# Optimization experiments

Measured on AMD Instinct MI355X. Metric: run time of the kernel, lower is better.

Reference implementation:

```python
import jax, jax.numpy as jnp
import numpy as np

B, T, C = 2, 2048, 2048
H, N = 32, 64
EPS_GN = 1e-5 * 8**2  # GroupNorm eps = 1e-5 * head_size_divisor**2


def setup_inputs() -> dict:
    key = jax.random.key(0)
    ks = iter(jax.random.split(key, 40))
    nk = lambda: next(ks)
    u = lambda shape: jax.random.uniform(nk(), shape, jnp.float32)
    n = lambda shape, s: jax.random.normal(nk(), shape, jnp.float32) * s
    return dict(
        x=jax.random.normal(nk(), (B, T, C), jnp.float32),
        v_first=jax.random.normal(nk(), (B, T, C), jnp.float32),
        x_r=u((1, 1, C)), x_w=u((1, 1, C)), x_k=u((1, 1, C)),
        x_v=u((1, 1, C)), x_a=u((1, 1, C)), x_g=u((1, 1, C)),
        w0=(jnp.linspace(-7.0, -2.0, C) + 0.5).reshape(1, 1, C).astype(jnp.float32),
        w1=n((C, 64), 0.02), w2=n((64, C), 0.1),
        a0=jnp.zeros((1, 1, C), jnp.float32), a1=n((C, 64), 0.02), a2=n((64, C), 0.1),
        v0=jnp.ones((1, 1, C), jnp.float32), v1=n((C, 32), 0.02), v2=n((32, C), 0.1),
        g1=n((C, 128), 0.02), g2=n((128, C), 0.1),
        k_k=jnp.full((1, 1, C), 0.85, jnp.float32),
        k_a=jnp.ones((1, 1, C), jnp.float32),
        r_k=n((H, N), 0.1),
        W_r=n((C, C), C ** -0.5), W_k=n((C, C), 0.1 * C ** -0.5),
        W_v=n((C, C), C ** -0.5), W_o=n((C, C), 0.02),
        gn_w=jnp.ones((C,), jnp.float32), gn_b=jnp.zeros((C,), jnp.float32),
    )


def _rwkv7(r, w, k, v, z, b):
    # all inputs [B,T,H,N]; state S [B,H,N_v,N_k] per head
    decay = jnp.exp(-jnp.exp(w))

    def step(S, xs):
        rt, dt, kt, vt, zt, bt = xs  # each [B,H,N]
        sa = jnp.einsum('bhij,bhj->bhi', S, zt)
        S = (S * dt[:, :, None, :]
             + sa[..., None] * bt[:, :, None, :]
             + vt[..., None] * kt[:, :, None, :])
        y = jnp.einsum('bhij,bhj->bhi', S, rt)
        return S, y

    xs = tuple(jnp.moveaxis(t, 1, 0) for t in (r, decay, k, v, z, b))
    S0 = jnp.zeros((r.shape[0], r.shape[2], N, N), r.dtype)
    _, ys = jax.lax.scan(step, S0, xs)
    return jnp.moveaxis(ys, 0, 1)  # [B,T,H,N]


def reference(x, v_first, x_r, x_w, x_k, x_v, x_a, x_g,
              w0, w1, w2, a0, a1, a2, v0, v1, v2, g1, g2,
              k_k, k_a, r_k, W_r, W_k, W_v, W_o, gn_w, gn_b):
    # time shift: x_{t-1} (zero at t=0) minus x
    xx = jnp.concatenate([jnp.zeros_like(x[:, :1]), x[:, :-1]], axis=1) - x
    xr = x + xx * x_r
    xw = x + xx * x_w
    xk = x + xx * x_k
    xv = x + xx * x_v
    xa = x + xx * x_a
    xg = x + xx * x_g

    r = xr @ W_r.T
    w = -jax.nn.softplus(-(w0 + jnp.tanh(xw @ w1) @ w2)) - 0.5  # log-decay in (-inf,-0.5)
    k = xk @ W_k.T
    v = xv @ W_v.T
    # layer_id != 0: blend with first-layer value
    v = v + (v_first - v) * jax.nn.sigmoid(v0 + (xv @ v1) @ v2)
    a = jax.nn.sigmoid(a0 + (xa @ a1) @ a2)
    g = jax.nn.sigmoid(xg @ g1) @ g2

    kk = (k * k_k).reshape(B, T, H, N)
    kk = kk / jnp.maximum(jnp.linalg.norm(kk, axis=-1, keepdims=True), 1e-12)
    k = k * (1.0 + (a - 1.0) * k_a)

    rh = r.reshape(B, T, H, N)
    kh = k.reshape(B, T, H, N)
    vh = v.reshape(B, T, H, N)
    ah = a.reshape(B, T, H, N)
    y = _rwkv7(rh, w.reshape(B, T, H, N), kh, vh, -kk, kk * ah)  # [B,T,H,N]

    # GroupNorm(H groups) over each head of each (b,t) row
    mu = y.mean(-1, keepdims=True)
    var = y.var(-1, keepdims=True)
    yn = ((y - mu) / jnp.sqrt(var + EPS_GN)).reshape(B, T, C) * gn_w + gn_b

    bonus = ((rh * kh * r_k).sum(-1, keepdims=True) * vh).reshape(B, T, C)
    out = ((yn + bonus) * g) @ W_o.T
    return (out, v_first)
```

## Files before the change

### kernel.cpp

```cpp
#include <hip/hip_runtime.h>
#include <stdint.h>

typedef unsigned short u16;
typedef unsigned int u32;

#define B_ 2
#define T_ 2048
#define C_ 2048
#define H_ 32
#define M_ (B_*T_)
static const size_t MC = (size_t)M_ * C_;

typedef __attribute__((ext_vector_type(8))) short s16x8;
typedef __attribute__((ext_vector_type(4))) float f32x4;

__device__ __forceinline__ u16 f2bf(float f) {
  union { float f; u32 u; } v; v.f = f;
  u32 r = v.u + 0x7FFFu + ((v.u >> 16) & 1u);
  return (u16)(r >> 16);
}
__device__ __forceinline__ float bits2f(u32 u) {
  union { u32 u; float f; } v; v.u = u; return v.f;
}
__device__ __forceinline__ float bf2f(u16 h) { return bits2f(((u32)h) << 16); }
__device__ __forceinline__ float sigm(float x) { return 1.0f / (1.0f + expf(-x)); }

__device__ __forceinline__ float wsum64(float x) {
  x += __shfl_xor(x, 32);
  x += __shfl_xor(x, 16);
  x += __shfl_xor(x, 8);
  x += __shfl_xor(x, 4);
  x += __shfl_xor(x, 2);
  x += __shfl_xor(x, 1);
  return x;
}

#define GL2LDS(g, l) __builtin_amdgcn_global_load_lds( \
    (const __attribute__((address_space(1))) u32*)(g), \
    (__attribute__((address_space(3))) u32*)(l), 16, 0, 0)

__global__ void __launch_bounds__(256) gemm128f(const u16* __restrict__ A, const u16* __restrict__ Bm,
                                                float* __restrict__ Cm, int M, int N, int K) {
  __shared__ u16 As[128 * 32];
  __shared__ u16 Bs[128 * 32];
  const int tid = threadIdx.x;
  const int w = tid >> 6, l = tid & 63;
  const int wm = w >> 1, wn = w & 1;
  const int bm = blockIdx.x, bn = blockIdx.y;

  const int row0 = tid >> 2, kq0 = tid & 3;
  const u16* ag0 = A + (size_t)(bm * 128 + row0) * K + kq0 * 8;
  const u16* ag1 = ag0 + (size_t)64 * K;
  const u16* bg0 = Bm + (size_t)(bn * 128 + row0) * K + kq0 * 8;
  const u16* bg1 = bg0 + (size_t)64 * K;
  u16* al0 = &As[w * 512];
  u16* al1 = &As[2048 + w * 512];
  u16* bl0 = &Bs[w * 512];
  u16* bl1 = &Bs[2048 + w * 512];

  const int lrow = l & 15, lko = (l >> 4) * 8;
  const u16* Ars = &As[(wm * 64 + lrow) * 32 + lko];
  const u16* Brs = &Bs[(wn * 64 + lrow) * 32 + lko];

  f32x4 acc[4][4] = {};
  for (int k0 = 0; k0 < K; k0 += 32) {
    __syncthreads();
    GL2LDS(ag0, al0); GL2LDS(ag1, al1);
    GL2LDS(bg0, bl0); GL2LDS(bg1, bl1);
    ag0 += 32; ag1 += 32; bg0 += 32; bg1 += 32;
    __syncthreads();
    s16x8 af[4], bf[4];
#pragma unroll
    for (int m = 0; m < 4; ++m) af[m] = *(const s16x8*)(Ars + m * 16 * 32);
#pragma unroll
    for (int n = 0; n < 4; ++n) bf[n] = *(const s16x8*)(Brs + n * 16 * 32);
#pragma unroll
    for (int m = 0; m < 4; ++m)
#pragma unroll
      for (int n = 0; n < 4; ++n)
        acc[m][n] = __builtin_amdgcn_mfma_f32_16x16x32_bf16(af[m], bf[n], acc[m][n], 0, 0, 0);
  }
  const int crow0 = bm * 128 + wm * 64 + (l >> 4) * 4;
  const int ccol0 = bn * 128 + wn * 64 + (l & 15);
#pragma unroll
  for (int m = 0; m < 4; ++m)
#pragma unroll
    for (int rr = 0; rr < 4; ++rr) {
      const int row = crow0 + m * 16 + rr;
      float* cp = Cm + (size_t)row * N + ccol0;
#pragma unroll
      for (int n = 0; n < 4; ++n) cp[n * 16] = acc[m][n][rr];
    }
}

struct GTab4 {
  const u16* A[4]; const u16* Bm[4]; u16* Cm[4]; int K[4];
};
__global__ void __launch_bounds__(256) gemm128z(GTab4 t, int M, int N) {
  __shared__ u16 As[128 * 32];
  __shared__ u16 Bs[128 * 32];
  const int z = blockIdx.z;
  const u16* A = t.A[z];
  const u16* Bm = t.Bm[z];
  u16* Cm = t.Cm[z];
  const int K = t.K[z];
  const int tid = threadIdx.x;
  const int w = tid >> 6, l = tid & 63;
  const int wm = w >> 1, wn = w & 1;
  const int bm = blockIdx.x, bn = blockIdx.y;

  const int row0 = tid >> 2, kq0 = tid & 3;
  const u16* ag0 = A + (size_t)(bm * 128 + row0) * K + kq0 * 8;
  const u16* ag1 = ag0 + (size_t)64 * K;
  const u16* bg0 = Bm + (size_t)(bn * 128 + row0) * K + kq0 * 8;
  const u16* bg1 = bg0 + (size_t)64 * K;
  u16* al0 = &As[w * 512];
  u16* al1 = &As[2048 + w * 512];
  u16* bl0 = &Bs[w * 512];
  u16* bl1 = &Bs[2048 + w * 512];

  const int lrow = l & 15, lko = (l >> 4) * 8;
  const u16* Ars = &As[(wm * 64 + lrow) * 32 + lko];
  const u16* Brs = &Bs[(wn * 64 + lrow) * 32 + lko];

  f32x4 acc[4][4] = {};
  for (int k0 = 0; k0 < K; k0 += 32) {
    __syncthreads();
    GL2LDS(ag0, al0); GL2LDS(ag1, al1);
    GL2LDS(bg0, bl0); GL2LDS(bg1, bl1);
    ag0 += 32; ag1 += 32; bg0 += 32; bg1 += 32;
    __syncthreads();
    s16x8 af[4], bf[4];
#pragma unroll
    for (int m = 0; m < 4; ++m) af[m] = *(const s16x8*)(Ars + m * 16 * 32);
#pragma unroll
    for (int n = 0; n < 4; ++n) bf[n] = *(const s16x8*)(Brs + n * 16 * 32);
#pragma unroll
    for (int m = 0; m < 4; ++m)
#pragma unroll
      for (int n = 0; n < 4; ++n)
        acc[m][n] = __builtin_amdgcn_mfma_f32_16x16x32_bf16(af[m], bf[n], acc[m][n], 0, 0, 0);
  }
  const int crow0 = bm * 128 + wm * 64 + (l >> 4) * 4;
  const int ccol0 = bn * 128 + wn * 64 + (l & 15);
#pragma unroll
  for (int m = 0; m < 4; ++m)
#pragma unroll
    for (int rr = 0; rr < 4; ++rr) {
      const int row = crow0 + m * 16 + rr;
      u16* cp = Cm + (size_t)row * N + ccol0;
#pragma unroll
      for (int n = 0; n < 4; ++n) cp[n * 16] = f2bf(acc[m][n][rr]);
    }
}

__global__ void __launch_bounds__(256) gemm_lora1(
    const u16* __restrict__ xwb, const u16* __restrict__ xab,
    const u16* __restrict__ xvb, const u16* __restrict__ xgb,
    const u16* __restrict__ w1t, const u16* __restrict__ a1t,
    const u16* __restrict__ v1t, const u16* __restrict__ g1t,
    float* __restrict__ hw, float* __restrict__ ha,
    float* __restrict__ hv, float* __restrict__ hg) {
  __shared__ u16 As[128 * 32];
  __shared__ u16 Bs[32 * 32];
  const int tid = threadIdx.x;
  const int w = tid >> 6, l = tid & 63;
  const int bm = blockIdx.x, g = blockIdx.y, z = blockIdx.z;

  const u16* A; const u16* Bm; float* Cm; int ldc, coloff;
  switch (g) {
    case 0:  A = xwb; Bm = w1t;             Cm = hw; ldc = 64;  coloff = 0;  break;
    case 1:  A = xwb; Bm = w1t + 32 * 2048; Cm = hw; ldc = 64;  coloff = 32; break;
    case 2:  A = xab; Bm = a1t;             Cm = ha; ldc = 64;  coloff = 0;  break;
    case 3:  A = xab; Bm = a1t + 32 * 2048; Cm = ha; ldc = 64;  coloff = 32; break;
    case 4:  A = xvb; Bm = v1t;             Cm = hv; ldc = 32;  coloff = 0;  break;
    default: {
      int gg = g - 5;
      A = xgb; Bm = g1t + (size_t)gg * 32 * 2048; Cm = hg; ldc = 128; coloff = gg * 32;
    }
  }
  A += z * 1024; Bm += z * 1024;
  Cm += (size_t)z * M_ * ldc;

  const int row0 = tid >> 2, kq0 = tid & 3;
  const u16* ag0 = A + (size_t)(bm * 128 + row0) * 2048 + kq0 * 8;
  const u16* ag1 = ag0 + (size_t)64 * 2048;
  u16* al0 = &As[w * 512];
  u16* al1 = &As[2048 + w * 512];
  const int bc = (w & 1) * 64 + l;
  const u16* bg0 = Bm + (size_t)(bc >> 2) * 2048 + (bc & 3) * 8;
  u16* bl0 = &Bs[(w & 1) * 512];

  const int lrow = l & 15, lko = (l >> 4) * 8;
  const u16* Ars = &As[(w * 32 + lrow) * 32 + lko];
  const u16* Brs = &Bs[lrow * 32 + lko];

  f32x4 acc[2][2] = {};
  for (int k0 = 0; k0 < 1024; k0 += 32) {
    __syncthreads();
    GL2LDS(ag0, al0); GL2LDS(ag1, al1);
    if (w < 2) GL2LDS(bg0, bl0);
    ag0 += 32; ag1 += 32; bg0 += 32;
    __syncthreads();
    s16x8 af[2], bf[2];
    af[0] = *(const s16x8*)(Ars);
    af[1] = *(const s16x8*)(Ars + 16 * 32);
    bf[0] = *(const s16x8*)(Brs);
    bf[1] = *(const s16x8*)(Brs + 16 * 32);
#pragma unroll
    for (int m = 0; m < 2; ++m)
#pragma unroll
      for (int n = 0; n < 2; ++n)
        acc[m][n] = __builtin_amdgcn_mfma_f32_16x16x32_bf16(af[m], bf[n], acc[m][n], 0, 0, 0);
  }
  const int crow0 = bm * 128 + w * 32 + (l >> 4) * 4;
  const int ccol0 = coloff + (l & 15);
#pragma unroll
  for (int m = 0; m < 2; ++m)
#pragma unroll
    for (int rr = 0; rr < 4; ++rr) {
      const int row = crow0 + m * 16 + rr;
      float* cp = Cm + (size_t)row * ldc + ccol0;
      cp[0] = acc[m][0][rr];
      cp[16] = acc[m][1][rr];
    }
}

__global__ void __launch_bounds__(256) act_lora(
    const float* __restrict__ hw, const float* __restrict__ ha,
    const float* __restrict__ hv, const float* __restrict__ hg,
    u16* __restrict__ hwb, u16* __restrict__ hab,
    u16* __restrict__ hvb, u16* __restrict__ hgb) {
  int gid = blockIdx.x * 256 + threadIdx.x;
  const int S0 = M_ * 64, S1 = M_ * 64, S2 = M_ * 32, S3 = M_ * 128;
  float v; u16* out; int idx;
  if (gid < S0) { idx = gid; v = tanhf(hw[idx] + hw[idx + S0]); out = hwb; }
  else if (gid < S0 + S1) { idx = gid - S0; v = ha[idx] + ha[idx + S1]; out = hab; }
  else if (gid < S0 + S1 + S2) { idx = gid - S0 - S1; v = hv[idx] + hv[idx + S2]; out = hvb; }
  else { idx = gid - S0 - S1 - S2; v = sigm(hg[idx] + hg[idx + S3]); out = hgb; }
  out[idx] = f2bf(v);
}

__global__ void __launch_bounds__(256) prep_mix(const float* __restrict__ x,
    const float* __restrict__ mr, const float* __restrict__ mw, const float* __restrict__ mk,
    const float* __restrict__ mv, const float* __restrict__ ma, const float* __restrict__ mg,
    u16* __restrict__ xrb, u16* __restrict__ xwb, u16* __restrict__ xkb,
    u16* __restrict__ xvb, u16* __restrict__ xab, u16* __restrict__ xgb) {
  int gid = blockIdx.x * 256 + threadIdx.x;
  int row = gid >> 8;
  int col = (gid & 255) << 3;
  size_t base = (size_t)row * C_ + col;
  float xv[8], dx[8];
  *(float4*)&xv[0] = *(const float4*)(x + base);
  *(float4*)&xv[4] = *(const float4*)(x + base + 4);
  if ((row & (T_ - 1)) == 0) {
#pragma unroll
    for (int j = 0; j < 8; ++j) dx[j] = -xv[j];
  } else {
    float xp[8];
    *(float4*)&xp[0] = *(const float4*)(x + base - C_);
    *(float4*)&xp[4] = *(const float4*)(x + base - C_ + 4);
#pragma unroll
    for (int j = 0; j < 8; ++j) dx[j] = xp[j] - xv[j];
  }
#define EMIT(dst, mixp) { \
    float4 m0 = *(const float4*)(mixp + col); \
    float4 m1 = *(const float4*)(mixp + col + 4); \
    float o0 = xv[0] + dx[0] * m0.x, o1 = xv[1] + dx[1] * m0.y; \
    float o2 = xv[2] + dx[2] * m0.z, o3 = xv[3] + dx[3] * m0.w; \
    float o4 = xv[4] + dx[4] * m1.x, o5 = xv[5] + dx[5] * m1.y; \
    float o6 = xv[6] + dx[6] * m1.z, o7 = xv[7] + dx[7] * m1.w; \
    uint4 pk; \
    pk.x = (u32)f2bf(o0) | ((u32)f2bf(o1) << 16); \
    pk.y = (u32)f2bf(o2) | ((u32)f2bf(o3) << 16); \
    pk.z = (u32)f2bf(o4) | ((u32)f2bf(o5) << 16); \
    pk.w = (u32)f2bf(o6) | ((u32)f2bf(o7) << 16); \
    *(uint4*)(dst + base) = pk; }
  EMIT(xrb, mr) EMIT(xwb, mw) EMIT(xkb, mk) EMIT(xvb, mv) EMIT(xab, ma) EMIT(xgb, mg)
#undef EMIT
}

__global__ void __launch_bounds__(256) convbf8x4(
    const float* __restrict__ i0, const float* __restrict__ i1,
    const float* __restrict__ i2, const float* __restrict__ i3,
    u16* __restrict__ o0, u16* __restrict__ o1, u16* __restrict__ o2, u16* __restrict__ o3) {
  const float* in; u16* out;
  switch (blockIdx.y) {
    case 0: in = i0; out = o0; break;
    case 1: in = i1; out = o1; break;
    case 2: in = i2; out = o2; break;
    default: in = i3; out = o3;
  }
  int gid = blockIdx.x * 256 + threadIdx.x;
  size_t b = (size_t)gid * 8;
  float4 a0 = *(const float4*)(in + b), a1 = *(const float4*)(in + b + 4);
  uint4 pk;
  pk.x = (u32)f2bf(a0.x) | ((u32)f2bf(a0.y) << 16);
  pk.y = (u32)f2bf(a0.z) | ((u32)f2bf(a0.w) << 16);
  pk.z = (u32)f2bf(a1.x) | ((u32)f2bf(a1.y) << 16);
  pk.w = (u32)f2bf(a1.z) | ((u32)f2bf(a1.w) << 16);
  *(uint4*)(out + b) = pk;
}

__global__ void __launch_bounds__(256) tconvbf8(
    const float* __restrict__ w1, const float* __restrict__ a1,
    const float* __restrict__ v1, const float* __restrict__ g1,
    const float* __restrict__ w2, const float* __restrict__ a2,
    const float* __restrict__ v2, const float* __restrict__ g2,
    u16* __restrict__ w1t, u16* __restrict__ a1t, u16* __restrict__ v1t, u16* __restrict__ g1t,
    u16* __restrict__ w2t, u16* __restrict__ a2t, u16* __restrict__ v2t, u16* __restrict__ g2t) {
  const float* in; u16* out; int R, Cc;
  switch (blockIdx.y) {
    case 0: in = w1; out = w1t; R = 2048; Cc = 64; break;
    case 1: in = a1; out = a1t; R = 2048; Cc = 64; break;
    case 2: in = v1; out = v1t; R = 2048; Cc = 32; break;
    case 3: in = g1; out = g1t; R = 2048; Cc = 128; break;
    case 4: in = w2; out = w2t; R = 64; Cc = 2048; break;
    case 5: in = a2; out = a2t; R = 64; Cc = 2048; break;
    case 6: in = v2; out = v2t; R = 32; Cc = 2048; break;
    default: in = g2; out = g2t; R = 128; Cc = 2048;
  }
  int gid = blockIdx.x * 256 + threadIdx.x;
  if (gid >= R * Cc) return;
  int i = gid % R, j = gid / R;
  out[gid] = f2bf(in[(size_t)i * Cc + j]);
}

__global__ void __launch_bounds__(256) scan_prep(
    const u16* __restrict__ rb, u16* __restrict__ kb, u16* __restrict__ vb,
    const u16* __restrict__ dwb, u16* __restrict__ dab, u16* __restrict__ dvbb,
    const float* __restrict__ v_first,
    const float* __restrict__ a0, const float* __restrict__ v0, const float* __restrict__ w0,
    const float* __restrict__ k_k, const float* __restrict__ k_a, const float* __restrict__ r_k,
    float* __restrict__ dec, u16* __restrict__ bonus) {
  int rh = blockIdx.x * 4 + (threadIdx.x >> 6);
  int n = threadIdx.x & 63;
  int h = rh & (H_ - 1);
  size_t idx = (size_t)rh * 64 + n;
  int c = h * 64 + n;
  float kv = bf2f(kb[idx]), dav = bf2f(dab[idx]), dwv = bf2f(dwb[idx]);
  float dvv = bf2f(dvbb[idx]), vv = bf2f(vb[idx]);
  float vf = v_first[idx], rv = bf2f(rb[idx]);
  float av = sigm(a0[c] + dav);
  float kkv = kv * k_k[c];
  float ss = wsum64(kkv * kkv);
  float kkn = kkv / fmaxf(sqrtf(ss), 1e-12f);
  float k2 = kv * (1.f + (av - 1.f) * k_a[c]);
  float w_ = w0[c] + dwv;
  float wl = -log1pf(expf(-w_)) - 0.5f;
  float decf = expf(-expf(wl));
  float sv = sigm(v0[c] + dvv);
  float v2 = vv + (vf - vv) * sv;
  float bp = wsum64(rv * k2 * r_k[c]);
  kb[idx] = f2bf(k2);
  vb[idx] = f2bf(v2);
  dab[idx] = f2bf(kkn * av);
  dvbb[idx] = f2bf(-kkn);
  dec[idx] = decf;
  bonus[idx] = f2bf(bp * v2);
}

__global__ void __launch_bounds__(256, 1) rwkv_scan(
    const u16* __restrict__ rb, const float* __restrict__ decb, const u16* __restrict__ kb,
    const u16* __restrict__ vb, const u16* __restrict__ zb, const u16* __restrict__ bbuf,
    float* __restrict__ yb) {
  __shared__ u16 Zt[16][72], Rt[16][72], Bt[16][72], Kt[16][72];
  __shared__ u16 BKT[64][40];
  __shared__ u16 SAVT[16][40];
  __shared__ u16 MK32[16][40];
  __shared__ u16 MRBK[16][40];
  __shared__ float Mb[16][20];
  __shared__ float basef[16][20];
  __shared__ float Ldec[16][68];
  __shared__ float cum[17][68];
  __shared__ float Sf[16][68];
  __shared__ u16 Sbf[16][72];

  const int tid = threadIdx.x;
  const int w = tid >> 6, l = tid & 63;
  const int bh = blockIdx.x >> 2;
  const int rblk = blockIdx.x & 3;
  const int bbx = bh >> 5, h = bh & 31;
  const int i0 = rblk * 16;
  const size_t headbase = ((size_t)bbx * T_ * H_ + h) * 64;

  for (int p = tid; p < 16 * 68; p += 256) ((float*)Sf)[p] = 0.f;
  for (int p = tid; p < 16 * 72; p += 256) ((u16*)Sbf)[p] = 0;
  for (int p = tid; p < 16 * 40; p += 256) { ((u16*)SAVT)[p] = 0; ((u16*)MK32)[p] = 0; }

  const int st_ = tid >> 4;
  const int sj = (tid & 15) * 4;
  const size_t g0 = headbase + (size_t)st_ * C_ + sj;

  uint2 cr, ck, cv, cz, cb; float4 cd;
  cr = *(const uint2*)(rb + g0);
  ck = *(const uint2*)(kb + g0);
  cv = *(const uint2*)(vb + g0);
  cz = *(const uint2*)(zb + g0);
  cb = *(const uint2*)(bbuf + g0);
  cd = *(const float4*)(decb + g0);

  *(float4*)&Ldec[st_][sj] = cd;
  __syncthreads();

  const int lrow = l & 15, lko = (l >> 4) * 8;

  for (int ch = 0; ch < T_ / 16; ++ch) {
    if (w == 0) {
      float dv[16];
#pragma unroll
      for (int t = 0; t < 16; ++t) dv[t] = Ldec[t][l];
      float c = 1.f;
      cum[0][l] = 1.f;
#pragma unroll
      for (int t = 0; t < 16; ++t) { c *= dv[t]; cum[t + 1][l] = c; }
    }
    __syncthreads();
    {
      float4 cp = *(const float4*)&cum[st_][sj];
      float4 cc = *(const float4*)&cum[st_ + 1][sj];
      float rv[4], kv[4], zv[4], bv[4];
      rv[0] = bf2f((u16)(cr.x & 0xffff)); rv[1] = bf2f((u16)(cr.x >> 16));
      rv[2] = bf2f((u16)(cr.y & 0xffff)); rv[3] = bf2f((u16)(cr.y >> 16));
      kv[0] = bf2f((u16)(ck.x & 0xffff)); kv[1] = bf2f((u16)(ck.x >> 16));
      kv[2] = bf2f((u16)(ck.y & 0xffff)); kv[3] = bf2f((u16)(ck.y >> 16));
      zv[0] = bf2f((u16)(cz.x & 0xffff)); zv[1] = bf2f((u16)(cz.x >> 16));
      zv[2] = bf2f((u16)(cz.y & 0xffff)); zv[3] = bf2f((u16)(cz.y >> 16));
      bv[0] = bf2f((u16)(cb.x & 0xffff)); bv[1] = bf2f((u16)(cb.x >> 16));
      bv[2] = bf2f((u16)(cb.y & 0xffff)); bv[3] = bf2f((u16)(cb.y >> 16));
      float cpv[4] = {cp.x, cp.y, cp.z, cp.w};
      float ccv[4] = {cc.x, cc.y, cc.z, cc.w};
      u16 zt4[4], rt4[4], bt4[4], kt4[4];
#pragma unroll
      for (int m = 0; m < 4; ++m) {
        float inv = 1.0f / ccv[m];
        zt4[m] = f2bf(zv[m] * cpv[m]);
        rt4[m] = f2bf(rv[m] * ccv[m]);
        bt4[m] = f2bf(bv[m] * inv);
        kt4[m] = f2bf(kv[m] * inv);
      }
      *(uint2*)&Zt[st_][sj] = *(uint2*)zt4;
      *(uint2*)&Rt[st_][sj] = *(uint2*)rt4;
      *(uint2*)&Bt[st_][sj] = *(uint2*)bt4;
      *(uint2*)&Kt[st_][sj] = *(uint2*)kt4;
#pragma unroll
      for (int m = 0; m < 4; ++m) {
        BKT[sj + m][st_] = bt4[m];
        BKT[sj + m][16 + st_] = kt4[m];
      }
      if ((sj >> 4) == rblk) {
        u16 vv4[4];
        vv4[0] = (u16)(cv.x & 0xffff); vv4[1] = (u16)(cv.x >> 16);
        vv4[2] = (u16)(cv.y & 0xffff); vv4[3] = (u16)(cv.y >> 16);
#pragma unroll
        for (int m = 0; m < 4; ++m) SAVT[(sj & 15) + m][16 + st_] = vv4[m];
      }
      if (ch + 1 < T_ / 16) {
        size_t g2 = g0 + (size_t)(ch + 1) * 16 * C_;
        cr = *(const uint2*)(rb + g2);
        ck = *(const uint2*)(kb + g2);
        cv = *(const uint2*)(vb + g2);
        cz = *(const uint2*)(zb + g2);
        cb = *(const uint2*)(bbuf + g2);
        cd = *(const float4*)(decb + g2);
      }
    }
    __syncthreads();
    f32x4 keep = {};
    {
      s16x8 a0f, a1f, b0f, b1f;
      if (w == 0 || w == 1) {
        a0f = *(const s16x8*)&Zt[lrow][lko];
        a1f = *(const s16x8*)&Zt[lrow][32 + lko];
      } else {
        a0f = *(const s16x8*)&Rt[lrow][lko];
        a1f = *(const s16x8*)&Rt[lrow][32 + lko];
      }
      if (w == 0 || w == 2) {
        b0f = *(const s16x8*)&Bt[lrow][lko];
        b1f = *(const s16x8*)&Bt[lrow][32 + lko];
      } else {
        b0f = *(const s16x8*)&Kt[lrow][lko];
        b1f = *(const s16x8*)&Kt[lrow][32 + lko];
      }
      f32x4 macc = {};
      macc = __builtin_amdgcn_mfma_f32_16x16x32_bf16(a0f, b0f, macc, 0, 0, 0);
      macc = __builtin_amdgcn_mfma_f32_16x16x32_bf16(a1f, b1f, macc, 0, 0, 0);
      const int s = l & 15;
#pragma unroll
      for (int rr = 0; rr < 4; ++rr) {
        int t = (l >> 4) * 4 + rr;
        float v = macc[rr];
        if (w == 0) Mb[t][s] = (s < t) ? v : 0.f;
        else if (w == 1) MK32[t][16 + s] = f2bf((s < t) ? v : 0.f);
        else if (w == 2) MRBK[t][s] = f2bf((s <= t) ? v : 0.f);
        else MRBK[t][16 + s] = f2bf((s <= t) ? v : 0.f);
      }
      if (w == 0 || w == 1) {
        s16x8 s0f = *(const s16x8*)&Sbf[lrow][lko];
        s16x8 s1f = *(const s16x8*)&Sbf[lrow][32 + lko];
        if (w == 0) {
          keep = __builtin_amdgcn_mfma_f32_16x16x32_bf16(a0f, s0f, keep, 0, 0, 0);
          keep = __builtin_amdgcn_mfma_f32_16x16x32_bf16(a1f, s1f, keep, 0, 0, 0);
        } else {
          s16x8 ra0 = *(const s16x8*)&Rt[lrow][lko];
          s16x8 ra1 = *(const s16x8*)&Rt[lrow][32 + lko];
          keep = __builtin_amdgcn_mfma_f32_16x16x32_bf16(ra0, s0f, keep, 0, 0, 0);
          keep = __builtin_amdgcn_mfma_f32_16x16x32_bf16(ra1, s1f, keep, 0, 0, 0);
        }
      }
    }
    __syncthreads();
    if (w == 0) {
      s16x8 af = *(const s16x8*)&MK32[lrow][lko];
      s16x8 bf = *(const s16x8*)&SAVT[lrow][lko];
      keep = __builtin_amdgcn_mfma_f32_16x16x32_bf16(af, bf, keep, 0, 0, 0);
      const int i = l & 15;
#pragma unroll
      for (int rr = 0; rr < 4; ++rr) basef[(l >> 4) * 4 + rr][i] = keep[rr];
      float bl[16];
#pragma unroll
      for (int t = 0; t < 16; ++t) bl[t] = basef[t][i];
      float sa[16];
#pragma unroll
      for (int b = 0; b < 4; ++b) {
        const int t0 = 4 * b;
        sa[t0] = bl[t0];
        sa[t0 + 1] = bl[t0 + 1] + Mb[t0 + 1][t0] * sa[t0];
        sa[t0 + 2] = bl[t0 + 2] + Mb[t0 + 2][t0] * sa[t0] + Mb[t0 + 2][t0 + 1] * sa[t0 + 1];
        sa[t0 + 3] = bl[t0 + 3] + Mb[t0 + 3][t0] * sa[t0] + Mb[t0 + 3][t0 + 1] * sa[t0 + 1]
                     + Mb[t0 + 3][t0 + 2] * sa[t0 + 2];
        if (b < 3) {
#pragma unroll
          for (int t = t0 + 4; t < 16; ++t) {
            f32x4 m4 = *(const f32x4*)&Mb[t][t0];
            bl[t] += (m4[0] * sa[t0] + m4[1] * sa[t0 + 1]) + (m4[2] * sa[t0 + 2] + m4[3] * sa[t0 + 3]);
          }
        }
      }
      if (l < 16) {
        u32* dst = (u32*)&SAVT[l][0];
#pragma unroll
        for (int m = 0; m < 8; ++m)
          dst[m] = (u32)f2bf(sa[2 * m]) | ((u32)f2bf(sa[2 * m + 1]) << 16);
      }
    }
    __syncthreads();
    if (w == 1) {
      s16x8 af = *(const s16x8*)&MRBK[lrow][lko];
      s16x8 bf = *(const s16x8*)&SAVT[lrow][lko];
      f32x4 yacc = __builtin_amdgcn_mfma_f32_16x16x32_bf16(af, bf, keep, 0, 0, 0);
#pragma unroll
      for (int rr = 0; rr < 4; ++rr) {
        int t = (l >> 4) * 4 + rr;
        yb[headbase + (size_t)(ch * 16 + t) * C_ + i0 + (l & 15)] = yacc[rr];
      }
    }
    {
      const int j0 = w * 16;
      s16x8 af = *(const s16x8*)&SAVT[lrow][lko];
      s16x8 bf = *(const s16x8*)&BKT[j0 + lrow][lko];
      f32x4 up = {};
      up = __builtin_amdgcn_mfma_f32_16x16x32_bf16(af, bf, up, 0, 0, 0);
      const int j = j0 + (l & 15);
      float cl = cum[16][j];
#pragma unroll
      for (int rr = 0; rr < 4; ++rr) {
        int i = (l >> 4) * 4 + rr;
        float sn = (Sf[i][j] + up[rr]) * cl;
        Sf[i][j] = sn;
        Sbf[i][j] = f2bf(sn);
      }
    }
    *(float4*)&Ldec[st_][sj] = cd;
    __syncthreads();
  }
}

__global__ void __launch_bounds__(256) gn_gg(
    const float* __restrict__ yb, const u16* __restrict__ bonus, const u16* __restrict__ gb,
    const float* __restrict__ gnw, const float* __restrict__ gnb,
    u16* __restrict__ ggb) {
  int rh = blockIdx.x * 4 + (threadIdx.x >> 6);
  int n = threadIdx.x & 63;
  int h = rh & (H_ - 1);
  size_t idx = (size_t)rh * 64 + n;
  int c = h * 64 + n;
  float y = yb[idx];
  float mu = wsum64(y) * (1.f / 64.f);
  float d = y - mu;
  float var = wsum64(d * d) * (1.f / 64.f);
  float yn = d * rsqrtf(var + 6.4e-4f) * gnw[c] + gnb[c];
  ggb[idx] = f2bf((yn + bf2f(bonus[idx])) * bf2f(gb[idx]));
}

extern "C" void kernel_launch(void* const* d_in, const int* in_sizes, int n_in,
                              void* d_out, int out_size, void* d_ws, size_t ws_size,
                              hipStream_t stream) {
  const float* x      = (const float*)d_in[0];
  const float* vfirst = (const float*)d_in[1];
  const float* x_r = (const float*)d_in[2];
  const float* x_w = (const float*)d_in[3];
  const float* x_k = (const float*)d_in[4];
  const float* x_v = (const float*)d_in[5];
  const float* x_a = (const float*)d_in[6];
  const float* x_g = (const float*)d_in[7];
  const float* w0  = (const float*)d_in[8];
  const float* w1  = (const float*)d_in[9];
  const float* w2  = (const float*)d_in[10];
  const float* a0  = (const float*)d_in[11];
  const float* a1  = (const float*)d_in[12];
  const float* a2  = (const float*)d_in[13];
  const float* v0  = (const float*)d_in[14];
  const float* v1  = (const float*)d_in[15];
  const float* v2  = (const float*)d_in[16];
  const float* g1  = (const float*)d_in[17];
  const float* g2  = (const float*)d_in[18];
  const float* k_k = (const float*)d_in[19];
  const float* k_a = (const float*)d_in[20];
  const float* r_k = (const float*)d_in[21];
  const float* W_r = (const float*)d_in[22];
  const float* W_k = (const float*)d_in[23];
  const float* W_v = (const float*)d_in[24];
  const float* W_o = (const float*)d_in[25];
  const float* gnw = (const float*)d_in[26];
  const float* gnb = (const float*)d_in[27];
  float* out = (float*)d_out;

  char* ws = (char*)d_ws;
  size_t off = 0;
  auto alloc = [&](size_t bytes) -> void* {
    void* p = ws + off;
    off += (bytes + 255) & ~(size_t)255;
    return p;
  };
  const size_t MCb2 = MC * 2;

  u16* xrb = (u16*)alloc(MCb2);
  u16* xwb = (u16*)alloc(MCb2);
  u16* xkb = (u16*)alloc(MCb2);
  u16* xvb = (u16*)alloc(MCb2);
  u16* xab = (u16*)alloc(MCb2);
  u16* xgb = (u16*)alloc(MCb2);
  u16* Wrb = (u16*)alloc((size_t)C_ * C_ * 2);
  u16* Wkb = (u16*)alloc((size_t)C_ * C_ * 2);
  u16* Wvb = (u16*)alloc((size_t)C_ * C_ * 2);
  u16* Wob = (u16*)alloc((size_t)C_ * C_ * 2);
  u16* w1t = (u16*)alloc((size_t)64 * C_ * 2);
  u16* a1t = (u16*)alloc((size_t)64 * C_ * 2);
  u16* v1t = (u16*)alloc((size_t)32 * C_ * 2);
  u16* g1t = (u16*)alloc((size_t)128 * C_ * 2);
  u16* w2t = (u16*)alloc((size_t)C_ * 64 * 2);
  u16* a2t = (u16*)alloc((size_t)C_ * 64 * 2);
  u16* v2t = (u16*)alloc((size_t)C_ * 32 * 2);
  u16* g2t = (u16*)alloc((size_t)C_ * 128 * 2);
  float* hw = (float*)alloc((size_t)M_ * 64 * 4 * 2);
  float* ha = (float*)alloc((size_t)M_ * 64 * 4 * 2);
  float* hv = (float*)alloc((size_t)M_ * 32 * 4 * 2);
  float* hg = (float*)alloc((size_t)M_ * 128 * 4 * 2);
  u16* hwb = (u16*)alloc((size_t)M_ * 64 * 2);
  u16* hab = (u16*)alloc((size_t)M_ * 64 * 2);
  u16* hvb = (u16*)alloc((size_t)M_ * 32 * 2);
  u16* hgb = (u16*)alloc((size_t)M_ * 128 * 2);
  u16* r_bf = (u16*)alloc(MCb2);
  u16* k_bf = (u16*)alloc(MCb2);
  u16* v_bf = (u16*)alloc(MCb2);
  float* dec = (float*)alloc(MC * 4);
  u16* bonus  = (u16*)alloc(MCb2);
  u16* dw_bf = xrb;
  u16* da_bf = xwb;
  u16* dv_bf = xkb;
  u16* g_bf  = xvb;
  float* yb  = (float*)xab;
  u16* ggb   = xrb;
  (void)ws_size; (void)in_sizes; (void)n_in; (void)out_size;

  dim3 blk(256);

  convbf8x4<<<dim3(C_ * C_ / 8 / 256, 4), blk, 0, stream>>>(W_r, W_k, W_v, W_o, Wrb, Wkb, Wvb, Wob);
  tconvbf8<<<dim3(1024, 8), blk, 0, stream>>>(w1, a1, v1, g1, w2, a2, v2, g2,
                                              w1t, a1t, v1t, g1t, w2t, a2t, v2t, g2t);

  prep_mix<<<(int)(MC / 8 / 256), blk, 0, stream>>>(x, x_r, x_w, x_k, x_v, x_a, x_g,
                                                    xrb, xwb, xkb, xvb, xab, xgb);
  hipMemcpyAsync(out + MC, vfirst, MC * sizeof(float), hipMemcpyDeviceToDevice, stream);

  {
    GTab4 t;
    t.A[0] = xrb; t.Bm[0] = Wrb; t.Cm[0] = r_bf; t.K[0] = 2048;
    t.A[1] = xkb; t.Bm[1] = Wkb; t.Cm[1] = k_bf; t.K[1] = 2048;
    t.A[2] = xvb; t.Bm[2] = Wvb; t.Cm[2] = v_bf; t.K[2] = 2048;
    t.A[3] = xrb; t.Bm[3] = Wrb; t.Cm[3] = r_bf; t.K[3] = 2048;
    gemm128z<<<dim3(M_ / 128, C_ / 128, 3), blk, 0, stream>>>(t, M_, C_);
  }

  gemm_lora1<<<dim3(M_ / 128, 9, 2), blk, 0, stream>>>(xwb, xab, xvb, xgb,
                                                       w1t, a1t, v1t, g1t,
                                                       hw, ha, hv, hg);

  act_lora<<<dim3(M_ * 288 / 256), blk, 0, stream>>>(hw, ha, hv, hg, hwb, hab, hvb, hgb);

  {
    GTab4 t;
    t.A[0] = hwb; t.Bm[0] = w2t; t.Cm[0] = dw_bf; t.K[0] = 64;
    t.A[1] = hab; t.Bm[1] = a2t; t.Cm[1] = da_bf; t.K[1] = 64;
    t.A[2] = hvb; t.Bm[2] = v2t; t.Cm[2] = dv_bf; t.K[2] = 32;
    t.A[3] = hgb; t.Bm[3] = g2t; t.Cm[3] = g_bf;  t.K[3] = 128;
    gemm128z<<<dim3(M_ / 128, C_ / 128, 4), blk, 0, stream>>>(t, M_, C_);
  }

  scan_prep<<<M_ * H_ / 4, blk, 0, stream>>>(r_bf, k_bf, v_bf, dw_bf, da_bf, dv_bf, vfirst,
                                             a0, v0, w0, k_k, k_a, r_k, dec, bonus);

  rwkv_scan<<<dim3(256), dim3(256), 0, stream>>>(r_bf, dec, k_bf, v_bf, dv_bf, da_bf, yb);

  gn_gg<<<M_ * H_ / 4, blk, 0, stream>>>(yb, bonus, g_bf, gnw, gnb, ggb);

  gemm128f<<<dim3(M_ / 128, C_ / 128), blk, 0, stream>>>(ggb, Wob, out, M_, C_, C_);
}
```

Baseline: 700.1 us.

## Run RWKV chunked scan with a single wavefront per block, dropping barriers

Rewrites the chunked scan kernel so each block is a single 64-lane wavefront. That wave does all the work the four waves used to split (the intra-chunk matrices, base/y MFMAs, and the state update across four column tiles), and every __syncthreads is replaced by a compiler memory fence. The aim is to remove the per-chunk block barriers that dominate this latency-bound sequential scan. In exchange each block does four times the serial work per chunk and holds more prefetch registers, and correctness relies on LDS ordering within one wave.

```diff
diff --git a/kernel.cpp b/kernel.cpp
--- a/kernel.cpp
+++ b/kernel.cpp
@@ -38,6 +38,10 @@
 #define GL2LDS(g, l) __builtin_amdgcn_global_load_lds( \
     (const __attribute__((address_space(1))) u32*)(g), \
     (__attribute__((address_space(3))) u32*)(l), 16, 0, 0)
+
+#define MFMA16(a, b, c) __builtin_amdgcn_mfma_f32_16x16x32_bf16((a), (b), (c), 0, 0, 0)
+
+#define LDSFENCE() asm volatile("" ::: "memory")
 
 __global__ void __launch_bounds__(256) gemm128f(const u16* __restrict__ A, const u16* __restrict__ Bm,
                                                 float* __restrict__ Cm, int M, int N, int K) {
@@ -78,7 +82,7 @@
     for (int m = 0; m < 4; ++m)
 #pragma unroll
       for (int n = 0; n < 4; ++n)
-        acc[m][n] = __builtin_amdgcn_mfma_f32_16x16x32_bf16(af[m], bf[n], acc[m][n], 0, 0, 0);
+        acc[m][n] = MFMA16(af[m], bf[n], acc[m][n]);
   }
   const int crow0 = bm * 128 + wm * 64 + (l >> 4) * 4;
   const int ccol0 = bn * 128 + wn * 64 + (l & 15);
@@ -139,7 +143,7 @@
     for (int m = 0; m < 4; ++m)
 #pragma unroll
       for (int n = 0; n < 4; ++n)
-        acc[m][n] = __builtin_amdgcn_mfma_f32_16x16x32_bf16(af[m], bf[n], acc[m][n], 0, 0, 0);
+        acc[m][n] = MFMA16(af[m], bf[n], acc[m][n]);
   }
   const int crow0 = bm * 128 + wm * 64 + (l >> 4) * 4;
   const int ccol0 = bn * 128 + wn * 64 + (l & 15);
@@ -211,7 +215,7 @@
     for (int m = 0; m < 2; ++m)
 #pragma unroll
       for (int n = 0; n < 2; ++n)
-        acc[m][n] = __builtin_amdgcn_mfma_f32_16x16x32_bf16(af[m], bf[n], acc[m][n], 0, 0, 0);
+        acc[m][n] = MFMA16(af[m], bf[n], acc[m][n]);
   }
   const int crow0 = bm * 128 + w * 32 + (l >> 4) * 4;
   const int ccol0 = coloff + (l & 15);
@@ -360,7 +364,7 @@
   bonus[idx] = f2bf(bp * v2);
 }
 
-__global__ void __launch_bounds__(256, 1) rwkv_scan(
+__global__ void __launch_bounds__(64, 1) rwkv_scan(
     const u16* __restrict__ rb, const float* __restrict__ decb, const u16* __restrict__ kb,
     const u16* __restrict__ vb, const u16* __restrict__ zb, const u16* __restrict__ bbuf,
     float* __restrict__ yb) {
@@ -376,37 +380,40 @@
   __shared__ float Sf[16][68];
   __shared__ u16 Sbf[16][72];
 
-  const int tid = threadIdx.x;
-  const int w = tid >> 6, l = tid & 63;
+  const int l = threadIdx.x;
   const int bh = blockIdx.x >> 2;
   const int rblk = blockIdx.x & 3;
   const int bbx = bh >> 5, h = bh & 31;
   const int i0 = rblk * 16;
   const size_t headbase = ((size_t)bbx * T_ * H_ + h) * 64;
 
-  for (int p = tid; p < 16 * 68; p += 256) ((float*)Sf)[p] = 0.f;
-  for (int p = tid; p < 16 * 72; p += 256) ((u16*)Sbf)[p] = 0;
-  for (int p = tid; p < 16 * 40; p += 256) { ((u16*)SAVT)[p] = 0; ((u16*)MK32)[p] = 0; }
-
-  const int st_ = tid >> 4;
-  const int sj = (tid & 15) * 4;
-  const size_t g0 = headbase + (size_t)st_ * C_ + sj;
-
-  uint2 cr, ck, cv, cz, cb; float4 cd;
-  cr = *(const uint2*)(rb + g0);
-  ck = *(const uint2*)(kb + g0);
-  cv = *(const uint2*)(vb + g0);
-  cz = *(const uint2*)(zb + g0);
-  cb = *(const uint2*)(bbuf + g0);
-  cd = *(const float4*)(decb + g0);
-
-  *(float4*)&Ldec[st_][sj] = cd;
-  __syncthreads();
+  for (int p = l; p < 16 * 68; p += 64) ((float*)Sf)[p] = 0.f;
+  for (int p = l; p < 16 * 72; p += 64) ((u16*)Sbf)[p] = 0;
+  for (int p = l; p < 16 * 40; p += 64) { ((u16*)SAVT)[p] = 0; ((u16*)MK32)[p] = 0; }
+  LDSFENCE();
+
+  const int tq = l >> 4;
+  const int sj = (l & 15) * 4;
+
+  uint2 cr[4], ck[4], cv[4], cz[4], cb[4]; float4 cd[4];
+#pragma unroll
+  for (int p = 0; p < 4; ++p) {
+    size_t g = headbase + (size_t)(tq + 4 * p) * C_ + sj;
+    cr[p] = *(const uint2*)(rb + g);
+    ck[p] = *(const uint2*)(kb + g);
+    cv[p] = *(const uint2*)(vb + g);
+    cz[p] = *(const uint2*)(zb + g);
+    cb[p] = *(const uint2*)(bbuf + g);
+    cd[p] = *(const float4*)(decb + g);
+  }
+#pragma unroll
+  for (int p = 0; p < 4; ++p) *(float4*)&Ldec[tq + 4 * p][sj] = cd[p];
+  LDSFENCE();
 
   const int lrow = l & 15, lko = (l >> 4) * 8;
 
   for (int ch = 0; ch < T_ / 16; ++ch) {
-    if (w == 0) {
+    {
       float dv[16];
 #pragma unroll
       for (int t = 0; t < 16; ++t) dv[t] = Ldec[t][l];
@@ -415,21 +422,23 @@
 #pragma unroll
       for (int t = 0; t < 16; ++t) { c *= dv[t]; cum[t + 1][l] = c; }
     }
-    __syncthreads();
-    {
-      float4 cp = *(const float4*)&cum[st_][sj];
-      float4 cc = *(const float4*)&cum[st_ + 1][sj];
+    LDSFENCE();
+#pragma unroll
+    for (int p = 0; p < 4; ++p) {
+      const int tp = tq + 4 * p;
+      float4 cp4 = *(const float4*)&cum[tp][sj];
+      float4 cc4 = *(const float4*)&cum[tp + 1][sj];
       float rv[4], kv[4], zv[4], bv[4];
-      rv[0] = bf2f((u16)(cr.x & 0xffff)); rv[1] = bf2f((u16)(cr.x >> 16));
-      rv[2] = bf2f((u16)(cr.y & 0xffff)); rv[3] = bf2f((u16)(cr.y >> 16));
-      kv[0] = bf2f((u16)(ck.x & 0xffff)); kv[1] = bf2f((u16)(ck.x >> 16));
-      kv[2] = bf2f((u16)(ck.y & 0xffff)); kv[3] = bf2f((u16)(ck.y >> 16));
-      zv[0] = bf2f((u16)(cz.x & 0xffff)); zv[1] = bf2f((u16)(cz.x >> 16));
-      zv[2] = bf2f((u16)(cz.y & 0xffff)); zv[3] = bf2f((u16)(cz.y >> 16));
-      bv[0] = bf2f((u16)(cb.x & 0xffff)); bv[1] = bf2f((u16)(cb.x >> 16));
-      bv[2] = bf2f((u16)(cb.y & 0xffff)); bv[3] = bf2f((u16)(cb.y >> 16));
-      float cpv[4] = {cp.x, cp.y, cp.z, cp.w};
-      float ccv[4] = {cc.x, cc.y, cc.z, cc.w};
+      rv[0] = bf2f((u16)(cr[p].x & 0xffff)); rv[1] = bf2f((u16)(cr[p].x >> 16));
+      rv[2] = bf2f((u16)(cr[p].y & 0xffff)); rv[3] = bf2f((u16)(cr[p].y >> 16));
+      kv[0] = bf2f((u16)(ck[p].x & 0xffff)); kv[1] = bf2f((u16)(ck[p].x >> 16));
+      kv[2] = bf2f((u16)(ck[p].y & 0xffff)); kv[3] = bf2f((u16)(ck[p].y >> 16));
+      zv[0] = bf2f((u16)(cz[p].x & 0xffff)); zv[1] = bf2f((u16)(cz[p].x >> 16));
+      zv[2] = bf2f((u16)(cz[p].y & 0xffff)); zv[3] = bf2f((u16)(cz[p].y >> 16));
+      bv[0] = bf2f((u16)(cb[p].x & 0xffff)); bv[1] = bf2f((u16)(cb[p].x >> 16));
+      bv[2] = bf2f((u16)(cb[p].y & 0xffff)); bv[3] = bf2f((u16)(cb[p].y >> 16));
+      float cpv[4] = {cp4.x, cp4.y, cp4.z, cp4.w};
+      float ccv[4] = {cc4.x, cc4.y, cc4.z, cc4.w};
       u16 zt4[4], rt4[4], bt4[4], kt4[4];
 #pragma unroll
       for (int m = 0; m < 4; ++m) {
@@ -439,85 +448,74 @@
         bt4[m] = f2bf(bv[m] * inv);
         kt4[m] = f2bf(kv[m] * inv);
       }
-      *(uint2*)&Zt[st_][sj] = *(uint2*)zt4;
-      *(uint2*)&Rt[st_][sj] = *(uint2*)rt4;
-      *(uint2*)&Bt[st_][sj] = *(uint2*)bt4;
-      *(uint2*)&Kt[st_][sj] = *(uint2*)kt4;
+      *(uint2*)&Zt[tp][sj] = *(uint2*)zt4;
+      *(uint2*)&Rt[tp][sj] = *(uint2*)rt4;
+      *(uint2*)&Bt[tp][sj] = *(uint2*)bt4;
+      *(uint2*)&Kt[tp][sj] = *(uint2*)kt4;
 #pragma unroll
       for (int m = 0; m < 4; ++m) {
-        BKT[sj + m][st_] = bt4[m];
-        BKT[sj + m][16 + st_] = kt4[m];
+        BKT[sj + m][tp] = bt4[m];
+        BKT[sj + m][16 + tp] = kt4[m];
       }
       if ((sj >> 4) == rblk) {
         u16 vv4[4];
-        vv4[0] = (u16)(cv.x & 0xffff); vv4[1] = (u16)(cv.x >> 16);
-        vv4[2] = (u16)(cv.y & 0xffff); vv4[3] = (u16)(cv.y >> 16);
-#pragma unroll
-        for (int m = 0; m < 4; ++m) SAVT[(sj & 15) + m][16 + st_] = vv4[m];
-      }
-      if (ch + 1 < T_ / 16) {
-        size_t g2 = g0 + (size_t)(ch + 1) * 16 * C_;
-        cr = *(const uint2*)(rb + g2);
-        ck = *(const uint2*)(kb + g2);
-        cv = *(const uint2*)(vb + g2);
-        cz = *(const uint2*)(zb + g2);
-        cb = *(const uint2*)(bbuf + g2);
-        cd = *(const float4*)(decb + g2);
-      }
-    }
-    __syncthreads();
-    f32x4 keep = {};
+        vv4[0] = (u16)(cv[p].x & 0xffff); vv4[1] = (u16)(cv[p].x >> 16);
+        vv4[2] = (u16)(cv[p].y & 0xffff); vv4[3] = (u16)(cv[p].y >> 16);
+#pragma unroll
+        for (int m = 0; m < 4; ++m) SAVT[(sj & 15) + m][16 + tp] = vv4[m];
+      }
+    }
+    if (ch + 1 < T_ / 16) {
+#pragma unroll
+      for (int p = 0; p < 4; ++p) {
+        size_t g = headbase + (size_t)(ch + 1) * 16 * C_ + (size_t)(tq + 4 * p) * C_ + sj;
+        cr[p] = *(const uint2*)(rb + g);
+        ck[p] = *(const uint2*)(kb + g);
+        cv[p] = *(const uint2*)(vb + g);
+        cz[p] = *(const uint2*)(zb + g);
+        cb[p] = *(const uint2*)(bbuf + g);
+        cd[p] = *(const float4*)(decb + g);
+      }
+    }
+    LDSFENCE();
+    f32x4 base1 = {}, y1 = {};
     {
-      s16x8 a0f, a1f, b0f, b1f;
-      if (w == 0 || w == 1) {
-        a0f = *(const s16x8*)&Zt[lrow][lko];
-        a1f = *(const s16x8*)&Zt[lrow][32 + lko];
-      } else {
-        a0f = *(const s16x8*)&Rt[lrow][lko];
-        a1f = *(const s16x8*)&Rt[lrow][32 + lko];
-      }
-      if (w == 0 || w == 2) {
-        b0f = *(const s16x8*)&Bt[lrow][lko];
-        b1f = *(const s16x8*)&Bt[lrow][32 + lko];
-      } else {
-        b0f = *(const s16x8*)&Kt[lrow][lko];
-        b1f = *(const s16x8*)&Kt[lrow][32 + lko];
-      }
-      f32x4 macc = {};
-      macc = __builtin_amdgcn_mfma_f32_16x16x32_bf16(a0f, b0f, macc, 0, 0, 0);
-      macc = __builtin_amdgcn_mfma_f32_16x16x32_bf16(a1f, b1f, macc, 0, 0, 0);
+      s16x8 za0 = *(const s16x8*)&Zt[lrow][lko];
+      s16x8 za1 = *(const s16x8*)&Zt[lrow][32 + lko];
+      s16x8 ra0 = *(const s16x8*)&Rt[lrow][lko];
+      s16x8 ra1 = *(const s16x8*)&Rt[lrow][32 + lko];
+      s16x8 bb0 = *(const s16x8*)&Bt[lrow][lko];
+      s16x8 bb1 = *(const s16x8*)&Bt[lrow][32 + lko];
+      s16x8 kk0 = *(const s16x8*)&Kt[lrow][lko];
+      s16x8 kk1 = *(const s16x8*)&Kt[lrow][32 + lko];
+      s16x8 sb0 = *(const s16x8*)&Sbf[lrow][lko];
+      s16x8 sb1 = *(const s16x8*)&Sbf[lrow][32 + lko];
+      f32x4 mb = {}, mk = {}, mrb = {}, mrk = {};
+      mb = MFMA16(za0, bb0, mb);   mb = MFMA16(za1, bb1, mb);
+      mk = MFMA16(za0, kk0, mk);   mk = MFMA16(za1, kk1, mk);
+      mrb = MFMA16(ra0, bb0, mrb); mrb = MFMA16(ra1, bb1, mrb);
+      mrk = MFMA16(ra0, kk0, mrk); mrk = MFMA16(ra1, kk1, mrk);
+      base1 = MFMA16(za0, sb0, base1); base1 = MFMA16(za1, sb1, base1);
+      y1 = MFMA16(ra0, sb0, y1);       y1 = MFMA16(ra1, sb1, y1);
       const int s = l & 15;
 #pragma unroll
       for (int rr = 0; rr < 4; ++rr) {
         int t = (l >> 4) * 4 + rr;
-        float v = macc[rr];
-        if (w == 0) Mb[t][s] = (s < t) ? v : 0.f;
-        else if (w == 1) MK32[t][16 + s] = f2bf((s < t) ? v : 0.f);
-        else if (w == 2) MRBK[t][s] = f2bf((s <= t) ? v : 0.f);
-        else MRBK[t][16 + s] = f2bf((s <= t) ? v : 0.f);
-      }
-      if (w == 0 || w == 1) {
-        s16x8 s0f = *(const s16x8*)&Sbf[lrow][lko];
-        s16x8 s1f = *(const s16x8*)&Sbf[lrow][32 + lko];
-        if (w == 0) {
-          keep = __builtin_amdgcn_mfma_f32_16x16x32_bf16(a0f, s0f, keep, 0, 0, 0);
-          keep = __builtin_amdgcn_mfma_f32_16x16x32_bf16(a1f, s1f, keep, 0, 0, 0);
-        } else {
-          s16x8 ra0 = *(const s16x8*)&Rt[lrow][lko];
-          s16x8 ra1 = *(const s16x8*)&Rt[lrow][32 + lko];
-          keep = __builtin_amdgcn_mfma_f32_16x16x32_bf16(ra0, s0f, keep, 0, 0, 0);
-          keep = __builtin_amdgcn_mfma_f32_16x16x32_bf16(ra1, s1f, keep, 0, 0, 0);
-        }
-      }
-    }
-    __syncthreads();
-    if (w == 0) {
+        Mb[t][s] = (s < t) ? mb[rr] : 0.f;
+        MK32[t][16 + s] = f2bf((s < t) ? mk[rr] : 0.f);
+        MRBK[t][s] = f2bf((s <= t) ? mrb[rr] : 0.f);
+        MRBK[t][16 + s] = f2bf((s <= t) ? mrk[rr] : 0.f);
+      }
+    }
+    LDSFENCE();
+    {
       s16x8 af = *(const s16x8*)&MK32[lrow][lko];
-      s16x8 bf = *(const s16x8*)&SAVT[lrow][lko];
-      keep = __builtin_amdgcn_mfma_f32_16x16x32_bf16(af, bf, keep, 0, 0, 0);
+      s16x8 bf_ = *(const s16x8*)&SAVT[lrow][lko];
+      base1 = MFMA16(af, bf_, base1);
       const int i = l & 15;
 #pragma unroll
-      for (int rr = 0; rr < 4; ++rr) basef[(l >> 4) * 4 + rr][i] = keep[rr];
+      for (int rr = 0; rr < 4; ++rr) basef[(l >> 4) * 4 + rr][i] = base1[rr];
+      LDSFENCE();
       float bl[16];
 #pragma unroll
       for (int t = 0; t < 16; ++t) bl[t] = basef[t][i];
@@ -545,35 +543,35 @@
           dst[m] = (u32)f2bf(sa[2 * m]) | ((u32)f2bf(sa[2 * m + 1]) << 16);
       }
     }
-    __syncthreads();
-    if (w == 1) {
+    LDSFENCE();
+    {
+      s16x8 savf = *(const s16x8*)&SAVT[lrow][lko];
       s16x8 af = *(const s16x8*)&MRBK[lrow][lko];
-      s16x8 bf = *(const s16x8*)&SAVT[lrow][lko];
-      f32x4 yacc = __builtin_amdgcn_mfma_f32_16x16x32_bf16(af, bf, keep, 0, 0, 0);
+      f32x4 yacc = MFMA16(af, savf, y1);
 #pragma unroll
       for (int rr = 0; rr < 4; ++rr) {
         int t = (l >> 4) * 4 + rr;
         yb[headbase + (size_t)(ch * 16 + t) * C_ + i0 + (l & 15)] = yacc[rr];
       }
-    }
-    {
-      const int j0 = w * 16;
-      s16x8 af = *(const s16x8*)&SAVT[lrow][lko];
-      s16x8 bf = *(const s16x8*)&BKT[j0 + lrow][lko];
-      f32x4 up = {};
-      up = __builtin_amdgcn_mfma_f32_16x16x32_bf16(af, bf, up, 0, 0, 0);
-      const int j = j0 + (l & 15);
-      float cl = cum[16][j];
-#pragma unroll
-      for (int rr = 0; rr < 4; ++rr) {
-        int i = (l >> 4) * 4 + rr;
-        float sn = (Sf[i][j] + up[rr]) * cl;
-        Sf[i][j] = sn;
-        Sbf[i][j] = f2bf(sn);
-      }
-    }
-    *(float4*)&Ldec[st_][sj] = cd;
-    __syncthreads();
+#pragma unroll
+      for (int jt = 0; jt < 4; ++jt) {
+        s16x8 bkf = *(const s16x8*)&BKT[jt * 16 + lrow][lko];
+        f32x4 up = {};
+        up = MFMA16(savf, bkf, up);
+        const int j = jt * 16 + (l & 15);
+        float cl = cum[16][j];
+#pragma unroll
+        for (int rr = 0; rr < 4; ++rr) {
+          int i = (l >> 4) * 4 + rr;
+          float sn = (Sf[i][j] + up[rr]) * cl;
+          Sf[i][j] = sn;
+          Sbf[i][j] = f2bf(sn);
+        }
+      }
+#pragma unroll
+      for (int p = 0; p < 4; ++p) *(float4*)&Ldec[tq + 4 * p][sj] = cd[p];
+    }
+    LDSFENCE();
   }
 }
 
@@ -712,7 +710,7 @@
   scan_prep<<<M_ * H_ / 4, blk, 0, stream>>>(r_bf, k_bf, v_bf, dw_bf, da_bf, dv_bf, vfirst,
                                              a0, v0, w0, k_k, k_a, r_k, dec, bonus);
 
-  rwkv_scan<<<dim3(256), dim3(256), 0, stream>>>(r_bf, dec, k_bf, v_bf, dv_bf, da_bf, yb);
+  rwkv_scan<<<dim3(256), dim3(64), 0, stream>>>(r_bf, dec, k_bf, v_bf, dv_bf, da_bf, yb);
 
   gn_gg<<<M_ * H_ / 4, blk, 0, stream>>>(yb, bonus, g_bf, gnw, gnb, ggb);
 
```

After: 885.5 us. 26.5% more time.
